# Kernel tuning notes

Hardware: AMD Instinct MI355X
Metric: run time of the kernel (lower is better)

## Reference

```python
import jax, jax.numpy as jnp
import numpy as np

NB_TF = 8
N_SEQ_TF = 2

# Concrete transform set (fixed magnitude 5 folded into constants), images in [0,1]

def _identity(v):
    return v

def _flip_lr(v):
    return v[..., ::-1]

def _flip_ud(v):
    return v[..., ::-1, :]

def _brightness(v):
    BRIGHT_FACTOR = 1.5  # mag 5 -> 1 + 5/10
    return jnp.clip(v * BRIGHT_FACTOR, 0.0, 1.0)

def _contrast(v):
    CONTRAST_FACTOR = 1.5
    mean = jnp.mean(v, axis=(-3, -2, -1), keepdims=True)  # per-image mean over C,H,W
    return jnp.clip((v - mean) * CONTRAST_FACTOR + mean, 0.0, 1.0)

def _solarize(v):
    THRESH = 0.5
    return jnp.where(v < THRESH, v, 1.0 - v)

def _invert(v):
    return 1.0 - v

def _posterize(v):
    LEVELS = 4.0  # mag 5 -> keep 2 bits
    return jnp.floor(v * LEVELS) / LEVELS

TFS = [_identity, _flip_lr, _flip_ud, _brightness, _contrast, _solarize, _invert, _posterize]


def setup_inputs() -> dict:
    key = jax.random.key(0)
    k1, k2, k3 = jax.random.split(key, 3)
    B, C, H, W = 128, 3, 224, 224
    x = jax.random.uniform(k1, (B, C, H, W), dtype=jnp.float32)
    prob = jax.random.uniform(k2, (NB_TF,), dtype=jnp.float32)  # learned routing param
    samples = jax.random.randint(k3, (N_SEQ_TF, B), 0, NB_TF, dtype=jnp.int32)
    return {"x": x, "prob": prob, "samples": samples}


def reference(x, prob, samples):
    # distrib is computed in the torch forward but only affects sampling (already
    # materialized in `samples`); recompute for faithfulness of the routing math.
    MIX = 0.5
    uniform = jax.nn.softmax(jnp.ones((NB_TF,), dtype=x.dtype))
    _distrib = jax.nn.softmax(MIX * prob + (1.0 - MIX) * uniform)  # noqa: F841

    out = x
    for step in range(samples.shape[0]):
        s = samples[step]  # [B] sampled TF index per image
        mask4 = s[:, None, None, None]  # broadcast over C,H,W
        y = jnp.zeros_like(out)
        # Equivalent of the boolean-mask gather/scatter dispatch: compute each
        # branch on the full batch and select per element (dense JAX analogue).
        for tf_idx, tf in enumerate(TFS):
            y = jnp.where(mask4 == tf_idx, tf(out), y)
        out = y
    return out
```

## Files before the change

kernel.cpp:

```cpp
#include <hip/hip_runtime.h>
#include <hip/hip_bf16.h>


#define B_    128
#define C_    3
#define H_    224
#define W_    224
#define N_ELEM (C_*H_*W_)
#define N4    (N_ELEM/4)
#define W4    (W_/4)
#define HW4   (H_*W4)
#define S_    32
#define CHUNK (N4/S_)
#define ABPI  21
#define APT   7

typedef float f32x4 __attribute__((ext_vector_type(4)));

__device__ __forceinline__ float apply_pw(float v, int tf, float mean) {
    switch (tf) {
        case 3: return fminf(fmaxf(v * 1.5f, 0.0f), 1.0f);
        case 4: return fminf(fmaxf((v - mean) * 1.5f + mean, 0.0f), 1.0f);
        case 5: return (v < 0.5f) ? v : (1.0f - v);
        case 6: return 1.0f - v;
        case 7: return floorf(v * 4.0f) * 0.25f;
        default: return v;
    }
}

__device__ __forceinline__ float2 block_reduce_sum2(float a, float b) {
    #pragma unroll
    for (int o = 32; o > 0; o >>= 1) {
        a += __shfl_down(a, o, 64);
        b += __shfl_down(b, o, 64);
    }
    __shared__ float2 smem[4];
    const int lane = threadIdx.x & 63, wid = threadIdx.x >> 6;
    __syncthreads();
    if (lane == 0) smem[wid] = make_float2(a, b);
    __syncthreads();
    float2 r;
    r.x = (smem[0].x + smem[1].x) + (smem[2].x + smem[3].x);
    r.y = (smem[0].y + smem[1].y) + (smem[2].y + smem[3].y);
    return r;
}

__global__ __launch_bounds__(256) void k_reduce(const float* __restrict__ x,
                                                const int* __restrict__ samples,
                                                float* __restrict__ ws) {
    const int img = blockIdx.x >> 5, blk = blockIdx.x & 31;
    const int t0 = samples[img], t1 = samples[B_ + img];
    if (!((t0 == 4) || (t1 == 4))) return;
    const bool need1 = (t1 == 4) && (t0 == 3 || t0 == 5 || t0 == 7);
    float* p0 = ws;
    float* p1 = ws + B_ * S_;
    const float4* xc = (const float4*)x + (size_t)img * N4 + blk * CHUNK;

    float a0 = 0.f, a1 = 0.f;
    for (int i = threadIdx.x; i < CHUNK; i += 256) {
        float4 v = xc[i];
        a0 += (v.x + v.y) + (v.z + v.w);
        if (need1) {
            a1 += apply_pw(v.x, t0, 0.f) + apply_pw(v.y, t0, 0.f)
                + apply_pw(v.z, t0, 0.f) + apply_pw(v.w, t0, 0.f);
        }
    }
    float2 r = block_reduce_sum2(a0, a1);
    if (threadIdx.x == 0) {
        p0[img * S_ + blk] = r.x;
        if (need1) p1[img * S_ + blk] = r.y;
    }
}

__global__ __launch_bounds__(256) void k_reduce2(const float* __restrict__ x,
                                                 const int* __restrict__ samples,
                                                 float* __restrict__ ws) {
    const int img = blockIdx.x >> 5, blk = blockIdx.x & 31;
    const int t0 = samples[img], t1 = samples[B_ + img];
    if (!(t0 == 4 && t1 == 4)) return;
    const float* p0 = ws;
    float* p1 = ws + B_ * S_;

    float s = 0.f;
    #pragma unroll
    for (int i = 0; i < S_; ++i) s += p0[img * S_ + i];
    const float m0 = s * (1.0f / N_ELEM);

    const float4* xc = (const float4*)x + (size_t)img * N4 + blk * CHUNK;
    float a1 = 0.f;
    for (int i = threadIdx.x; i < CHUNK; i += 256) {
        float4 v = xc[i];
        a1 += apply_pw(v.x, 4, m0) + apply_pw(v.y, 4, m0)
            + apply_pw(v.z, 4, m0) + apply_pw(v.w, 4, m0);
    }
    float2 r = block_reduce_sum2(a1, 0.f);
    if (threadIdx.x == 0) p1[img * S_ + blk] = r.x;
}

__global__ __launch_bounds__(256) void k_apply(const float* __restrict__ x,
                                               const int* __restrict__ samples,
                                               const float* __restrict__ ws,
                                               float* __restrict__ out) {
    const int img = blockIdx.x / ABPI;
    const int t0 = samples[img], t1 = samples[B_ + img];
    const float* p0 = ws;
    const float* p1 = ws + B_ * S_;

    __shared__ float means[2];
    if (threadIdx.x == 0) {
        float m0 = 0.f, m1 = 0.f;
        if (t0 == 4 || t1 == 4) {
            float s = 0.f;
            #pragma unroll
            for (int i = 0; i < S_; ++i) s += p0[img * S_ + i];
            m0 = s * (1.0f / N_ELEM);
        }
        if (t1 == 4) {
            if (t0 < 3)       m1 = m0;
            else if (t0 == 6) m1 = 1.0f - m0;
            else {
                float s = 0.f;
                #pragma unroll
                for (int i = 0; i < S_; ++i) s += p1[img * S_ + i];
                m1 = s * (1.0f / N_ELEM);
            }
        }
        means[0] = m0; means[1] = m1;
    }
    __syncthreads();
    const float m0 = means[0], m1 = means[1];

    const bool fw = (t0 == 1) ^ (t1 == 1);
    const bool fh = (t0 == 2) ^ (t1 == 2);

    const float4* xi = (const float4*)x + (size_t)img * N4;
    f32x4* oi = (f32x4*)out + (size_t)img * N4;
    const int base = (blockIdx.x % ABPI) * (256 * APT) + threadIdx.x;

    #pragma unroll
    for (int k = 0; k < APT; ++k) {
        const int idx = base + k * 256;
        const int c = idx / HW4, rem = idx % HW4;
        const int h = rem / W4, wq = rem % W4;
        const int hs  = fh ? (H_ - 1 - h)  : h;
        const int wqs = fw ? (W4 - 1 - wq) : wq;
        float4 v = xi[c * HW4 + hs * W4 + wqs];
        if (fw) { float t = v.x; v.x = v.w; v.w = t; t = v.y; v.y = v.z; v.z = t; }
        f32x4 r;
        r.x = apply_pw(apply_pw(v.x, t0, m0), t1, m1);
        r.y = apply_pw(apply_pw(v.y, t0, m0), t1, m1);
        r.z = apply_pw(apply_pw(v.z, t0, m0), t1, m1);
        r.w = apply_pw(apply_pw(v.w, t0, m0), t1, m1);
        __builtin_nontemporal_store(r, &oi[idx]);
    }
}

extern "C" void kernel_launch(void* const* d_in, const int* in_sizes, int n_in,
                              void* d_out, int out_size, void* d_ws, size_t ws_size,
                              hipStream_t stream) {
    const float* x       = (const float*)d_in[0];
    const int*   samples = (const int*)d_in[2];
    float*       out     = (float*)d_out;
    float*       ws      = (float*)d_ws;

    k_reduce <<<B_ * S_,   256, 0, stream>>>(x, samples, ws);
    k_reduce2<<<B_ * S_,   256, 0, stream>>>(x, samples, ws);
    k_apply  <<<B_ * ABPI, 256, 0, stream>>>(x, samples, ws, out);
}
```

Baseline: 151.2 us.

## Fold second contrast-mean reduction into apply kernel, dropping k_reduce2 launch

Removes the separate k_reduce2 kernel that computed the second-step contrast mean for images where both sampled transforms are contrast. In the apply kernel, each of the 21 blocks for such an image now redundantly reduces the whole image to get that mean before applying. This saves one kernel launch and its per-image block overhead. The cost is a full-image read repeated 21 times for those images, about 1/64 of the batch.

```diff
diff --git a/kernel.cpp b/kernel.cpp
--- a/kernel.cpp
+++ b/kernel.cpp
@@ -72,31 +72,6 @@
     }
 }
 
-__global__ __launch_bounds__(256) void k_reduce2(const float* __restrict__ x,
-                                                 const int* __restrict__ samples,
-                                                 float* __restrict__ ws) {
-    const int img = blockIdx.x >> 5, blk = blockIdx.x & 31;
-    const int t0 = samples[img], t1 = samples[B_ + img];
-    if (!(t0 == 4 && t1 == 4)) return;
-    const float* p0 = ws;
-    float* p1 = ws + B_ * S_;
-
-    float s = 0.f;
-    #pragma unroll
-    for (int i = 0; i < S_; ++i) s += p0[img * S_ + i];
-    const float m0 = s * (1.0f / N_ELEM);
-
-    const float4* xc = (const float4*)x + (size_t)img * N4 + blk * CHUNK;
-    float a1 = 0.f;
-    for (int i = threadIdx.x; i < CHUNK; i += 256) {
-        float4 v = xc[i];
-        a1 += apply_pw(v.x, 4, m0) + apply_pw(v.y, 4, m0)
-            + apply_pw(v.z, 4, m0) + apply_pw(v.w, 4, m0);
-    }
-    float2 r = block_reduce_sum2(a1, 0.f);
-    if (threadIdx.x == 0) p1[img * S_ + blk] = r.x;
-}
-
 __global__ __launch_bounds__(256) void k_apply(const float* __restrict__ x,
                                                const int* __restrict__ samples,
                                                const float* __restrict__ ws,
@@ -105,35 +80,51 @@
     const int t0 = samples[img], t1 = samples[B_ + img];
     const float* p0 = ws;
     const float* p1 = ws + B_ * S_;
+    const float4* xi = (const float4*)x + (size_t)img * N4;
 
-    __shared__ float means[2];
-    if (threadIdx.x == 0) {
-        float m0 = 0.f, m1 = 0.f;
-        if (t0 == 4 || t1 == 4) {
-            float s = 0.f;
-            #pragma unroll
-            for (int i = 0; i < S_; ++i) s += p0[img * S_ + i];
-            m0 = s * (1.0f / N_ELEM);
+    float m0 = 0.f, m1 = 0.f;
+    if (t0 == 4 && t1 == 4) {
+        float s = 0.f;
+        #pragma unroll
+        for (int i = 0; i < S_; ++i) s += p0[img * S_ + i];
+        m0 = s * (1.0f / N_ELEM);
+        float a = 0.f;
+        for (int i = threadIdx.x; i < N4; i += 256) {
+            float4 v = xi[i];
+            a += apply_pw(v.x, 4, m0) + apply_pw(v.y, 4, m0)
+               + apply_pw(v.z, 4, m0) + apply_pw(v.w, 4, m0);
         }
-        if (t1 == 4) {
-            if (t0 < 3)       m1 = m0;
-            else if (t0 == 6) m1 = 1.0f - m0;
-            else {
+        float2 r = block_reduce_sum2(a, 0.f);
+        m1 = r.x * (1.0f / N_ELEM);
+    } else {
+        __shared__ float means[2];
+        if (threadIdx.x == 0) {
+            float a0 = 0.f, a1 = 0.f;
+            if (t0 == 4 || t1 == 4) {
                 float s = 0.f;
                 #pragma unroll
-                for (int i = 0; i < S_; ++i) s += p1[img * S_ + i];
-                m1 = s * (1.0f / N_ELEM);
+                for (int i = 0; i < S_; ++i) s += p0[img * S_ + i];
+                a0 = s * (1.0f / N_ELEM);
             }
+            if (t1 == 4) {
+                if (t0 < 3)       a1 = a0;
+                else if (t0 == 6) a1 = 1.0f - a0;
+                else {
+                    float s = 0.f;
+                    #pragma unroll
+                    for (int i = 0; i < S_; ++i) s += p1[img * S_ + i];
+                    a1 = s * (1.0f / N_ELEM);
+                }
+            }
+            means[0] = a0; means[1] = a1;
         }
-        means[0] = m0; means[1] = m1;
+        __syncthreads();
+        m0 = means[0]; m1 = means[1];
     }
-    __syncthreads();
-    const float m0 = means[0], m1 = means[1];
 
     const bool fw = (t0 == 1) ^ (t1 == 1);
     const bool fh = (t0 == 2) ^ (t1 == 2);
 
-    const float4* xi = (const float4*)x + (size_t)img * N4;
     f32x4* oi = (f32x4*)out + (size_t)img * N4;
     const int base = (blockIdx.x % ABPI) * (256 * APT) + threadIdx.x;
 
@@ -163,7 +154,6 @@
     float*       out     = (float*)d_out;
     float*       ws      = (float*)d_ws;
 
-    k_reduce <<<B_ * S_,   256, 0, stream>>>(x, samples, ws);
-    k_reduce2<<<B_ * S_,   256, 0, stream>>>(x, samples, ws);
-    k_apply  <<<B_ * ABPI, 256, 0, stream>>>(x, samples, ws, out);
+    k_reduce<<<B_ * S_,   256, 0, stream>>>(x, samples, ws);
+    k_apply <<<B_ * ABPI, 256, 0, stream>>>(x, samples, ws, out);
 }
```

New measurement: 183.7 us. 21.5% more time.
